# Optimization experiments

Hardware: AMD Instinct MI355X
Metric: run time of the kernel (lower is better)

Reference implementation:

```python
import jax, jax.numpy as jnp
import numpy as np
import math

EPS = 1e-6          # eps for safe cumprod / clamping
CHUNK = 4           # chunk_size w
SHARP = 1.0         # sharpening_factor
NOISE_STD = 1.0
N_HEADS = 4
ADIM = 512


def moving_sum(x, back, forward):
    """Windowed running sum over last axis: out[k] = sum_{j=k-back}^{k+forward} x[j].
    Equivalent to the conv1d trick in the original (all-ones filter)."""
    k = x.shape[-1]
    pad = [(0, 0)] * (x.ndim - 1) + [(back, forward)]
    c = jnp.cumsum(jnp.pad(x, pad), axis=-1)
    c0 = jnp.concatenate([jnp.zeros_like(c[..., :1]), c], axis=-1)
    w = back + forward
    return c0[..., w + 1: w + 1 + k] - c0[..., :k]


def setup_inputs() -> dict:
    rng = jax.random.key(0)
    ks = jax.random.split(rng, 12)
    B, qlen, klen, kdim, qdim, adim = 8, 256, 2048, 512, 512, ADIM
    s = 0.02
    return {
        "key_enc": jax.random.normal(ks[0], (B, klen, kdim), jnp.float32),
        "query":   jax.random.normal(ks[1], (B, qlen, qdim), jnp.float32),
        "noise":   jax.random.normal(ks[2], (B, qlen, klen), jnp.float32),
        # monotonic energy params
        "Wk_m": jax.random.normal(ks[3], (kdim, adim), jnp.float32) * s,
        "bk_m": jnp.zeros((adim,), jnp.float32),
        "Wq_m": jax.random.normal(ks[4], (qdim, adim), jnp.float32) * s,
        "bq_m": jnp.zeros((adim,), jnp.float32),
        "r":    jnp.array([-4.0], jnp.float32),
        # chunkwise energy params (multi-head)
        "Wk_c": jax.random.normal(ks[5], (kdim, adim), jnp.float32) * s,
        "bk_c": jnp.zeros((adim,), jnp.float32),
        "Wq_c": jax.random.normal(ks[6], (qdim, adim), jnp.float32) * s,
        "bq_c": jnp.zeros((adim,), jnp.float32),
    }


def _mocha_beta(key_enc, query, noise, Wk_m, bk_m, Wq_m, bq_m, r,
                Wk_c, bk_c, Wq_c, bq_c):
    B, klen, _ = key_enc.shape
    qlen = query.shape[1]
    H = N_HEADS
    dk = ADIM // H
    scale = math.sqrt(ADIM)

    # --- monotonic energy (single head): [B, qlen, klen]
    k_m = key_enc @ Wk_m + bk_m
    q_m = query @ Wq_m + bq_m
    e_mono = jnp.einsum('bqa,bka->bqk', q_m, k_m) / scale + r[0]

    # --- p_choose with additive gaussian noise (encourages discreteness)
    p_choose = jax.nn.sigmoid(e_mono + noise * NOISE_STD)  # [B,q,k]

    # --- safe cumprod of (1 - p) via exclusive cumsum in log space
    log1mp = jnp.log(jnp.clip(1.0 - p_choose, EPS, 1.0))
    cumprod_1mp = jnp.exp(jnp.cumsum(log1mp, axis=-1) - log1mp)  # exclusive

    # --- monotonic alpha recurrence over query steps (parallel-mode MoChA)
    aw0 = jnp.zeros((B, klen), jnp.float32).at[:, 0].set(1.0)

    def step(aw_prev, inp):
        p_i, cp_i = inp  # [B, klen]
        alpha_i = p_i * cp_i * jnp.cumsum(
            aw_prev / jnp.clip(cp_i, EPS, 1.0), axis=-1)
        return alpha_i, alpha_i

    xs = (jnp.swapaxes(p_choose, 0, 1), jnp.swapaxes(cumprod_1mp, 0, 1))
    _, alpha_q = jax.lax.scan(step, aw0, xs)          # [q, B, k]
    alpha = jnp.swapaxes(alpha_q, 0, 1)                # [B, q, k]

    # --- chunkwise energy (multi-head): [B, H, q, k]
    k_c = (key_enc @ Wk_c + bk_c).reshape(B, klen, H, dk)
    q_c = (query @ Wq_c + bq_c).reshape(B, qlen, H, dk)
    e_chunk = jnp.einsum('bqhd,bkhd->bhqk', q_c, k_c) / scale

    # --- efficient chunkwise attention (clipped-logit moving-sum softmax)
    e = e_chunk - jnp.max(e_chunk, axis=3, keepdims=True)
    softmax_exp = jnp.maximum(jnp.exp(e), 1e-5)
    denom = moving_sum(softmax_exp, back=CHUNK - 1, forward=0)
    beta = softmax_exp * moving_sum(
        alpha[:, None] * SHARP / denom, back=0, forward=CHUNK - 1)
    return beta  # [B, H, q, k]


def reference(key_enc, query, noise, Wk_m, bk_m, Wq_m, bq_m, r,
              Wk_c, bk_c, Wq_c, bq_c):
    return _mocha_beta(key_enc, query, noise, Wk_m, bk_m, Wq_m, bq_m, r,
                       Wk_c, bk_c, Wq_c, bq_c)
```

## Files before the change

### kernel.cpp

```cpp
#include <hip/hip_runtime.h>
#include <math.h>

#define BATCH   8
#define QLEN    256
#define KLEN    2048
#define KDIM    512
#define ADIMC   512
#define NHEADS  4
#define DKH     128
#define CHUNKW  4

static constexpr float INV_SCALE = 0.04419417382415922f;
static constexpr float EPSV = 1e-6f;

typedef __attribute__((ext_vector_type(8))) short bf16x8;
typedef __attribute__((ext_vector_type(4))) float f32x4;

__device__ __forceinline__ unsigned short f2bf(float f) {
    unsigned u = __builtin_bit_cast(unsigned, f);
    u += 0x7fffu + ((u >> 16) & 1u);
    return (unsigned short)(u >> 16);
}

__device__ __forceinline__ void lds_barrier() {
    __asm__ volatile("s_waitcnt lgkmcnt(0)\n\ts_barrier" ::: "memory");
}

__device__ __forceinline__ void gload_lds16(const void* g, void* l) {
    __builtin_amdgcn_global_load_lds(
        (const __attribute__((address_space(1))) void*)g,
        (__attribute__((address_space(3))) void*)l, 16, 0, 0);
}

#define NKXB (BATCH * KLEN * KDIM / 4 / 256)
#define NQXB (BATCH * QLEN * KDIM / 4 / 256)
__global__ __launch_bounds__(256) void prep(
    const float* __restrict__ key_enc, const float* __restrict__ query,
    const float* __restrict__ Wk_m, const float* __restrict__ Wk_c,
    const float* __restrict__ Wq_m, const float* __restrict__ Wq_c,
    unsigned short* __restrict__ kx, unsigned short* __restrict__ qx,
    unsigned short* __restrict__ WTk, unsigned short* __restrict__ WTq)
{
    __shared__ float tile[32][33];
    const int gb = blockIdx.x;
    const int tid = threadIdx.x;

    if (gb < NKXB + NQXB) {
        const float* x = (gb < NKXB) ? key_enc : query;
        unsigned short* y = (gb < NKXB) ? kx : qx;
        const int i = (gb < NKXB ? gb : gb - NKXB) * 256 + tid;
        float4 v = ((const float4*)x)[i];
        ushort4 o;
        o.x = f2bf(v.x); o.y = f2bf(v.y); o.z = f2bf(v.z); o.w = f2bf(v.w);
        ((ushort4*)y)[i] = o;
        return;
    }
    const int t = gb - NKXB - NQXB;
    const int which = t >> 8;
    const int tt = t & 255;
    const int bx = tt & 15, byy = tt >> 4;
    const float* W = (which == 0) ? Wk_m : (which == 1) ? Wk_c
                   : (which == 2) ? Wq_m : Wq_c;
    unsigned short* WT = (which == 0) ? WTk
                       : (which == 1) ? WTk + (size_t)512 * KDIM
                       : (which == 2) ? WTq : WTq + (size_t)512 * KDIM;
    const int tx = tid & 31, ty = tid >> 5;
    const int k0 = byy * 32, n0 = bx * 32;
    #pragma unroll
    for (int i = 0; i < 32; i += 8)
        tile[ty + i][tx] = W[(size_t)(k0 + ty + i) * KDIM + n0 + tx];
    __syncthreads();
    #pragma unroll
    for (int i = 0; i < 32; i += 8)
        WT[(size_t)(n0 + ty + i) * KDIM + k0 + tx] = f2bf(tile[tx][ty + i]);
}

template<int KSTEPS>
__device__ __forceinline__ void mfma_nt_staged(
    const unsigned short* __restrict__ A, const unsigned short* __restrict__ B,
    int lda, int ldb, int bm, int bn,
    unsigned short* AsLDS, unsigned short* BsLDS, f32x4 acc[4][4])
{
    const int t = threadIdx.x;
    const int wv = t >> 6, ln = t & 63;
    const int r = ln & 15, quad = ln >> 4;
    const int wm = (wv >> 1) * 64, wn = (wv & 1) * 64;
    const int srow = wv * 16 + (ln >> 2);
    const int scol = (ln & 3) * 8;

    for (int ks = 0; ks < KSTEPS; ++ks) {
        const int k0 = ks * 32;
        #pragma unroll
        for (int j = 0; j < 2; ++j) {
            gload_lds16(A + (size_t)(bm + j * 64 + srow) * lda + k0 + scol,
                        AsLDS + (size_t)(j * 64 + wv * 16) * 32);
            gload_lds16(B + (size_t)(bn + j * 64 + srow) * ldb + k0 + scol,
                        BsLDS + (size_t)(j * 64 + wv * 16) * 32);
        }
        __syncthreads();
        bf16x8 af[4], bg[4];
        #pragma unroll
        for (int f = 0; f < 4; ++f)
            af[f] = *(const bf16x8*)(AsLDS + (size_t)(wm + f * 16 + r) * 32 + quad * 8);
        #pragma unroll
        for (int f = 0; f < 4; ++f)
            bg[f] = *(const bf16x8*)(BsLDS + (size_t)(wn + f * 16 + r) * 32 + quad * 8);
        #pragma unroll
        for (int i = 0; i < 4; ++i)
            #pragma unroll
            for (int j2 = 0; j2 < 4; ++j2)
                acc[i][j2] = __builtin_amdgcn_mfma_f32_16x16x32_bf16(
                    af[i], bg[j2], acc[i][j2], 0, 0, 0);
        __syncthreads();
    }
}

__device__ __forceinline__ void zero_acc(f32x4 acc[4][4]) {
    #pragma unroll
    for (int i = 0; i < 4; ++i)
        #pragma unroll
        for (int j = 0; j < 4; ++j)
            acc[i][j] = f32x4{0.f, 0.f, 0.f, 0.f};
}

__global__ __launch_bounds__(256) void proj_mfma(
    const unsigned short* __restrict__ kx, const unsigned short* __restrict__ qx,
    const unsigned short* __restrict__ WTk, const unsigned short* __restrict__ WTq,
    const float* __restrict__ bk_m, const float* __restrict__ bk_c,
    const float* __restrict__ bq_m, const float* __restrict__ bq_c,
    unsigned short* __restrict__ kproj, unsigned short* __restrict__ qproj)
{
    __shared__ unsigned short As[128 * 32];
    __shared__ unsigned short Bs[128 * 32];
    const int by = blockIdx.y;
    const unsigned short *A, *WT;
    unsigned short* C;
    const float *bm_, *bc_;
    int bm;
    if (by < 128) { A = kx; WT = WTk; C = kproj; bm_ = bk_m; bc_ = bk_c; bm = by * 128; }
    else          { A = qx; WT = WTq; C = qproj; bm_ = bq_m; bc_ = bq_c; bm = (by - 128) * 128; }
    const int bn = blockIdx.x * 128;
    f32x4 acc[4][4]; zero_acc(acc);
    mfma_nt_staged<16>(A, WT, KDIM, KDIM, bm, bn, As, Bs, acc);
    const int wv = threadIdx.x >> 6, ln = threadIdx.x & 63;
    const int r = ln & 15, quad = ln >> 4;
    const int m0 = bm + (wv >> 1) * 64, n0 = bn + (wv & 1) * 64;
    #pragma unroll
    for (int j = 0; j < 4; ++j) {
        const int n = n0 + j * 16 + r;
        const float bv = (n < 512) ? bm_[n] : bc_[n - 512];
        #pragma unroll
        for (int i = 0; i < 4; ++i) {
            #pragma unroll
            for (int reg = 0; reg < 4; ++reg) {
                const int m = m0 + i * 16 + quad * 4 + reg;
                C[(size_t)m * 1024 + n] = f2bf(acc[i][j][reg] + bv);
            }
        }
    }
}

__global__ __launch_bounds__(256) void pchoose_mfma(
    const unsigned short* __restrict__ qp, const unsigned short* __restrict__ kp,
    const float* __restrict__ noise, const float* __restrict__ rp,
    float* __restrict__ p)
{
    __shared__ unsigned short As[128 * 32];
    __shared__ unsigned short Bs[128 * 32];
    const int b = blockIdx.z;
    const unsigned short* A = qp + (size_t)b * QLEN * 1024;
    const unsigned short* B = kp + (size_t)b * KLEN * 1024;
    const int bm = blockIdx.y * 128, bn = blockIdx.x * 128;
    f32x4 acc[4][4]; zero_acc(acc);
    mfma_nt_staged<16>(A, B, 1024, 1024, bm, bn, As, Bs, acc);
    const int wv = threadIdx.x >> 6, ln = threadIdx.x & 63;
    const int r = ln & 15, quad = ln >> 4;
    const int m0 = bm + (wv >> 1) * 64, n0 = bn + (wv & 1) * 64;
    const float rv = rp[0];
    #pragma unroll
    for (int i = 0; i < 4; ++i) {
        #pragma unroll
        for (int reg = 0; reg < 4; ++reg) {
            const int q = m0 + i * 16 + quad * 4 + reg;
            const size_t rowoff = ((size_t)b * QLEN + q) * KLEN;
            #pragma unroll
            for (int j = 0; j < 4; ++j) {
                const int k = n0 + j * 16 + r;
                const float e = acc[i][j][reg] * INV_SCALE + rv + noise[rowoff + k];
                p[rowoff + k] = __builtin_amdgcn_rcpf(1.0f + __expf(-e));
            }
        }
    }
}

__device__ __forceinline__ float wave_incl_scan(float x)
{
#define DPP_ADD(ctrl, rmask, bctrl)                                            \
    { int _t = __builtin_amdgcn_update_dpp(0, __builtin_bit_cast(int, x),      \
                                           ctrl, rmask, 0xf, bctrl);           \
      x += __builtin_bit_cast(float, _t); }
    DPP_ADD(0x111, 0xf, true)
    DPP_ADD(0x112, 0xf, true)
    DPP_ADD(0x114, 0xf, true)
    DPP_ADD(0x118, 0xf, true)
    DPP_ADD(0x142, 0xa, false)
    DPP_ADD(0x143, 0xc, false)
#undef DPP_ADD
    return x;
}

__global__ __launch_bounds__(256) void cumprod_mr(
    const float* __restrict__ p, float* __restrict__ mArr, float* __restrict__ rArr)
{
    const size_t row = blockIdx.x;
    const float* pr = p + row * KLEN;
    float* mr = mArr + row * KLEN;
    float* rr = rArr + row * KLEN;
    const int tid = threadIdx.x;
    const int lane = tid & 63, wid = tid >> 6;
    __shared__ float waveTot[4];

    float4 v0 = *(const float4*)(pr + tid * 8);
    float4 v1 = *(const float4*)(pr + tid * 8 + 4);
    float pv[8] = {v0.x, v0.y, v0.z, v0.w, v1.x, v1.y, v1.z, v1.w};
    float excl[8];
    float run = 0.0f;
    #pragma unroll
    for (int j = 0; j < 8; ++j) {
        float l = __logf(fminf(fmaxf(1.0f - pv[j], EPSV), 1.0f));
        excl[j] = run;
        run += l;
    }
    float s = wave_incl_scan(run);
    if (lane == 63) waveTot[wid] = s;
    __syncthreads();
    float wex = 0.0f;
    for (int w = 0; w < wid; ++w) wex += waveTot[w];
    const float texcl = wex + s - run;

    float mv[8], rv[8];
    #pragma unroll
    for (int j = 0; j < 8; ++j) {
        const float cpv = __expf(texcl + excl[j]);
        mv[j] = pv[j] * cpv;
        rv[j] = __builtin_amdgcn_rcpf(fminf(fmaxf(cpv, EPSV), 1.0f));
    }
    *(float4*)(mr + tid * 8)     = *(float4*)&mv[0];
    *(float4*)(mr + tid * 8 + 4) = *(float4*)&mv[4];
    *(float4*)(rr + tid * 8)     = *(float4*)&rv[0];
    *(float4*)(rr + tid * 8 + 4) = *(float4*)&rv[4];
}

__global__ __launch_bounds__(256, 1) void alpha_echunk(
    const float* __restrict__ mArr, const float* __restrict__ rArr,
    float* __restrict__ alpha,
    const unsigned short* __restrict__ qp, const unsigned short* __restrict__ kp,
    float* __restrict__ out)
{
    __shared__ __align__(16) char smem[98304];
    const int bid = blockIdx.x;
    const int tid = threadIdx.x;

    if (bid < BATCH) {
        __builtin_amdgcn_s_setprio(1);
        float (*wt)[4] = (float (*)[4])smem;
        const int lane = tid & 63, wid = tid >> 6;
        const float* mrow = mArr + (size_t)bid * QLEN * KLEN + tid * 8;
        const float* rrow = rArr + (size_t)bid * QLEN * KLEN + tid * 8;
        float* arow = alpha + (size_t)bid * QLEN * KLEN + tid * 8;

        float aw0 = 0.f, aw1 = 0.f, aw2 = 0.f, aw3 = 0.f;
        float aw4 = 0.f, aw5 = 0.f, aw6 = 0.f, aw7 = 0.f;
        if (tid == 0) aw0 = 1.0f;

        float4 mA0 = *(const float4*)(mrow);
        float4 mA1 = *(const float4*)(mrow + 4);
        float4 rA0 = *(const float4*)(rrow);
        float4 rA1 = *(const float4*)(rrow + 4);
        float4 mB0 = *(const float4*)(mrow + KLEN);
        float4 mB1 = *(const float4*)(mrow + KLEN + 4);
        float4 rB0 = *(const float4*)(rrow + KLEN);
        float4 rB1 = *(const float4*)(rrow + KLEN + 4);

#define ASTEP(I, M0, M1, R0, R1)                                               \
    {                                                                          \
        const int i_ = (I);                                                    \
        float4 mc0 = M0, mc1 = M1, rc0 = R0, rc1 = R1;                         \
        const int rn_ = (i_ + 2 < QLEN) ? (i_ + 2) : (QLEN - 1);               \
        M0 = *(const float4*)(mrow + (size_t)rn_ * KLEN);                      \
        M1 = *(const float4*)(mrow + (size_t)rn_ * KLEN + 4);                  \
        R0 = *(const float4*)(rrow + (size_t)rn_ * KLEN);                      \
        R1 = *(const float4*)(rrow + (size_t)rn_ * KLEN + 4);                  \
        float run = 0.0f, i0, i1, i2, i3, i4, i5, i6, i7;                      \
        run = fmaf(aw0, rc0.x, run); i0 = run;                                 \
        run = fmaf(aw1, rc0.y, run); i1 = run;                                 \
        run = fmaf(aw2, rc0.z, run); i2 = run;                                 \
        run = fmaf(aw3, rc0.w, run); i3 = run;                                 \
        run = fmaf(aw4, rc1.x, run); i4 = run;                                 \
        run = fmaf(aw5, rc1.y, run); i5 = run;                                 \
        run = fmaf(aw6, rc1.z, run); i6 = run;                                 \
        run = fmaf(aw7, rc1.w, run); i7 = run;                                 \
        float tot = wave_incl_scan(run);                                       \
        if (lane == 63) wt[i_ & 1][wid] = tot;                                 \
        lds_barrier();                                                         \
        float base = tot - run;                                                \
        float4 w0 = *(const float4*)&wt[i_ & 1][0];                            \
        if (wid > 0) base += w0.x;                                             \
        if (wid > 1) base += w0.y;                                             \
        if (wid > 2) base += w0.z;                                             \
        aw0 = mc0.x * (base + i0);                                             \
        aw1 = mc0.y * (base + i1);                                             \
        aw2 = mc0.z * (base + i2);                                             \
        aw3 = mc0.w * (base + i3);                                             \
        aw4 = mc1.x * (base + i4);                                             \
        aw5 = mc1.y * (base + i5);                                             \
        aw6 = mc1.z * (base + i6);                                             \
        aw7 = mc1.w * (base + i7);                                             \
        float4 ov0; ov0.x = aw0; ov0.y = aw1; ov0.z = aw2; ov0.w = aw3;        \
        float4 ov1; ov1.x = aw4; ov1.y = aw5; ov1.z = aw6; ov1.w = aw7;        \
        *(float4*)(arow + (size_t)i_ * KLEN)     = ov0;                        \
        *(float4*)(arow + (size_t)i_ * KLEN + 4) = ov1;                        \
    }

        for (int io = 0; io < QLEN; io += 2) {
            ASTEP(io + 0, mA0, mA1, rA0, rA1)
            ASTEP(io + 1, mB0, mB1, rB0, rB1)
        }
#undef ASTEP
        __builtin_amdgcn_s_setprio(0);
        return;
    }

    const int v = bid - BATCH;
    const int z = v >> 5;
    const int by = (v >> 4) & 1;
    const int bx = v & 15;
    const int b = z >> 2, h = z & 3;
    unsigned short* As = (unsigned short*)smem;
    unsigned short* Bs = (unsigned short*)(smem + 8192);
    const unsigned short* A = qp + (size_t)b * QLEN * 1024 + 512 + h * DKH;
    const unsigned short* B = kp + (size_t)b * KLEN * 1024 + 512 + h * DKH;
    const int bm = by * 128, bn = bx * 128;

    const int wv = tid >> 6, ln = tid & 63;
    const int r = ln & 15, quad = ln >> 4;
    const int wm = (wv >> 1) * 64, wn = (wv & 1) * 64;
    const int srow = wv * 16 + (ln >> 2);
    const int scol = (ln & 3) * 8;

    f32x4 acc[4][4]; zero_acc(acc);
    for (int ks = 0; ks < 4; ++ks) {
        const int k0 = ks * 32;
        #pragma unroll
        for (int j = 0; j < 2; ++j) {
            gload_lds16(A + (size_t)(bm + j * 64 + srow) * 1024 + k0 + scol,
                        As + (size_t)(j * 64 + wv * 16) * 32);
            gload_lds16(B + (size_t)(bn + j * 64 + srow) * 1024 + k0 + scol,
                        Bs + (size_t)(j * 64 + wv * 16) * 32);
        }
        __syncthreads();
        bf16x8 af[4], bg[4];
        #pragma unroll
        for (int f = 0; f < 4; ++f)
            af[f] = *(const bf16x8*)(As + (size_t)(wm + f * 16 + r) * 32 + quad * 8);
        #pragma unroll
        for (int f = 0; f < 4; ++f)
            bg[f] = *(const bf16x8*)(Bs + (size_t)(wn + f * 16 + r) * 32 + quad * 8);
        #pragma unroll
        for (int i = 0; i < 4; ++i)
            #pragma unroll
            for (int j2 = 0; j2 < 4; ++j2)
                acc[i][j2] = __builtin_amdgcn_mfma_f32_16x16x32_bf16(
                    af[i], bg[j2], acc[i][j2], 0, 0, 0);
        __syncthreads();
    }
    {
        const int m0 = bm + (wv >> 1) * 64, n0 = bn + (wv & 1) * 64;
        #pragma unroll
        for (int i = 0; i < 4; ++i) {
            #pragma unroll
            for (int reg = 0; reg < 4; ++reg) {
                const int q = m0 + i * 16 + quad * 4 + reg;
                const size_t rowoff = ((size_t)z * QLEN + q) * KLEN;
                #pragma unroll
                for (int j = 0; j < 4; ++j) {
                    const int k = n0 + j * 16 + r;
                    out[rowoff + k] = acc[i][j][reg] * INV_SCALE;
                }
            }
        }
    }
}

__global__ __launch_bounds__(256) void beta_kernel(
    float* __restrict__ eo, const float* __restrict__ alpha)
{
    __shared__ float sse[KLEN + 3];
    __shared__ float su[KLEN + 3];
    __shared__ float wmax[4];

    const int tid = threadIdx.x;
    const int lane = tid & 63, wid = tid >> 6;
    const int row = blockIdx.x;
    const int q = row & (QLEN - 1);
    const int b = row >> 10;
    float* erow = eo + (size_t)row * KLEN;
    const float* arow = alpha + ((size_t)b * QLEN + q) * KLEN;

    if (tid < 3) { sse[tid] = 0.0f; su[KLEN + tid] = 0.0f; }

    float ev[8];
    float lm = -INFINITY;
    #pragma unroll
    for (int j = 0; j < 8; ++j) {
        const int k = tid + 256 * j;
        ev[j] = erow[k];
        lm = fmaxf(lm, ev[j]);
    }
    #pragma unroll
    for (int off = 32; off > 0; off >>= 1) lm = fmaxf(lm, __shfl_xor(lm, off));
    if (lane == 0) wmax[wid] = lm;
    __syncthreads();
    const float mx = fmaxf(fmaxf(wmax[0], wmax[1]), fmaxf(wmax[2], wmax[3]));

    #pragma unroll
    for (int j = 0; j < 8; ++j) {
        const int k = tid + 256 * j;
        sse[k + 3] = fmaxf(__expf(ev[j] - mx), 1e-5f);
    }
    __syncthreads();

    #pragma unroll
    for (int j = 0; j < 8; ++j) {
        const int k = tid + 256 * j;
        const float denom = sse[k + 3] + sse[k + 2] + sse[k + 1] + sse[k];
        su[k] = arow[k] * __builtin_amdgcn_rcpf(denom);
    }
    __syncthreads();

    #pragma unroll
    for (int j = 0; j < 8; ++j) {
        const int k = tid + 256 * j;
        erow[k] = sse[k + 3] * (su[k] + su[k + 1] + su[k + 2] + su[k + 3]);
    }
}

extern "C" void kernel_launch(void* const* d_in, const int* in_sizes, int n_in,
                              void* d_out, int out_size, void* d_ws, size_t ws_size,
                              hipStream_t stream)
{
    (void)in_sizes; (void)n_in; (void)out_size; (void)ws_size;
    const float* key_enc = (const float*)d_in[0];
    const float* query   = (const float*)d_in[1];
    const float* noise   = (const float*)d_in[2];
    const float* Wk_m    = (const float*)d_in[3];
    const float* bk_m    = (const float*)d_in[4];
    const float* Wq_m    = (const float*)d_in[5];
    const float* bq_m    = (const float*)d_in[6];
    const float* rp      = (const float*)d_in[7];
    const float* Wk_c    = (const float*)d_in[8];
    const float* bk_c    = (const float*)d_in[9];
    const float* Wq_c    = (const float*)d_in[10];
    const float* bq_c    = (const float*)d_in[11];
    float* out = (float*)d_out;

    char* w = (char*)d_ws;
    unsigned short* kx    = (unsigned short*)w; w += (size_t)BATCH * KLEN * KDIM * 2;
    unsigned short* qx    = (unsigned short*)w; w += (size_t)BATCH * QLEN * KDIM * 2;
    unsigned short* WTk   = (unsigned short*)w; w += (size_t)1024 * KDIM * 2;
    unsigned short* WTq   = (unsigned short*)w; w += (size_t)1024 * KDIM * 2;
    unsigned short* kproj = (unsigned short*)w; w += (size_t)BATCH * KLEN * 1024 * 2;
    unsigned short* qproj = (unsigned short*)w; w += (size_t)BATCH * QLEN * 1024 * 2;
    float* p_alpha = (float*)w; w += (size_t)BATCH * QLEN * KLEN * 4;
    float* mArr    = (float*)w; w += (size_t)BATCH * QLEN * KLEN * 4;
    float* rArr    = (float*)w;

    hipLaunchKernelGGL(prep, dim3(NKXB + NQXB + 1024), dim3(256), 0, stream,
                       key_enc, query, Wk_m, Wk_c, Wq_m, Wq_c,
                       kx, qx, WTk, WTq);

    hipLaunchKernelGGL(proj_mfma, dim3(8, BATCH * KLEN / 128 + BATCH * QLEN / 128),
                       dim3(256), 0, stream,
                       kx, qx, WTk, WTq, bk_m, bk_c, bq_m, bq_c, kproj, qproj);

    hipLaunchKernelGGL(pchoose_mfma, dim3(KLEN / 128, QLEN / 128, BATCH), dim3(256), 0, stream,
                       qproj, kproj, noise, rp, p_alpha);

    hipLaunchKernelGGL(cumprod_mr, dim3(BATCH * QLEN), dim3(256), 0, stream,
                       p_alpha, mArr, rArr);

    hipLaunchKernelGGL(alpha_echunk, dim3(BATCH + KLEN / 128 * QLEN / 128 * BATCH * NHEADS),
                       dim3(256), 0, stream,
                       mArr, rArr, p_alpha, qproj, kproj, out);

    hipLaunchKernelGGL(beta_kernel, dim3(BATCH * NHEADS * QLEN), dim3(256), 0, stream,
                       out, p_alpha);
}
```

Measured before the change: 296.6 us.

## Widen alpha scan to 512 threads and software-pipeline the cross-wave prefix

The sequential alpha recurrence now runs with 512 threads, each holding 4 elements instead of 8. The scan is restructured so the block-level carry for step i is computed in step i-1 (a second wave scan publishes next-step partial sums to LDS), leaving one barrier per step with the slot read hoisted ahead. The GEMM blocks now launch 512 threads, and only the first 256 do any work. The intent is to shorten the serial per-step critical path. The cost is extra arithmetic and a second wave scan per step, and the GEMM part carries idle waves that lower occupancy.

```diff
diff --git a/kernel.cpp b/kernel.cpp
--- a/kernel.cpp
+++ b/kernel.cpp
@@ -251,7 +251,7 @@
     *(float4*)(rr + tid * 8 + 4) = *(float4*)&rv[4];
 }
 
-__global__ __launch_bounds__(256, 1) void alpha_echunk(
+__global__ __launch_bounds__(512, 1) void alpha_echunk(
     const float* __restrict__ mArr, const float* __restrict__ rArr,
     float* __restrict__ alpha,
     const unsigned short* __restrict__ qp, const unsigned short* __restrict__ kp,
@@ -263,68 +263,82 @@
 
     if (bid < BATCH) {
         __builtin_amdgcn_s_setprio(1);
-        float (*wt)[4] = (float (*)[4])smem;
+        float* slots = (float*)smem;
         const int lane = tid & 63, wid = tid >> 6;
-        const float* mrow = mArr + (size_t)bid * QLEN * KLEN + tid * 8;
-        const float* rrow = rArr + (size_t)bid * QLEN * KLEN + tid * 8;
-        float* arow = alpha + (size_t)bid * QLEN * KLEN + tid * 8;
-
-        float aw0 = 0.f, aw1 = 0.f, aw2 = 0.f, aw3 = 0.f;
-        float aw4 = 0.f, aw5 = 0.f, aw6 = 0.f, aw7 = 0.f;
-        if (tid == 0) aw0 = 1.0f;
-
-        float4 mA0 = *(const float4*)(mrow);
-        float4 mA1 = *(const float4*)(mrow + 4);
-        float4 rA0 = *(const float4*)(rrow);
-        float4 rA1 = *(const float4*)(rrow + 4);
-        float4 mB0 = *(const float4*)(mrow + KLEN);
-        float4 mB1 = *(const float4*)(mrow + KLEN + 4);
-        float4 rB0 = *(const float4*)(rrow + KLEN);
-        float4 rB1 = *(const float4*)(rrow + KLEN + 4);
-
-#define ASTEP(I, M0, M1, R0, R1)                                               \
+        const float* mrow = mArr + (size_t)bid * QLEN * KLEN + tid * 4;
+        const float* rrow = rArr + (size_t)bid * QLEN * KLEN + tid * 4;
+        float* arow = alpha + (size_t)bid * QLEN * KLEN + tid * 4;
+
+        float4 uP = *(const float4*)(rrow);
+        float4 mA = *(const float4*)(mrow);
+        float4 rA = *(const float4*)(rrow + KLEN);
+        float4 mB = *(const float4*)(mrow + KLEN);
+        float4 rB = *(const float4*)(rrow + 2 * KLEN);
+        float4 sP;
+        sP.x = (tid == 0) ? 1.0f : 0.0f; sP.y = 0.f; sP.z = 0.f; sP.w = 0.f;
+        float Cw = 0.0f;
+
+        if (tid < 16) slots[tid] = 0.0f;
+        lds_barrier();
+        if (tid == 0) slots[0] = uP.x;
+        lds_barrier();
+
+#define ASTEP(I, M, R)                                                         \
     {                                                                          \
         const int i_ = (I);                                                    \
-        float4 mc0 = M0, mc1 = M1, rc0 = R0, rc1 = R1;                         \
-        const int rn_ = (i_ + 2 < QLEN) ? (i_ + 2) : (QLEN - 1);               \
-        M0 = *(const float4*)(mrow + (size_t)rn_ * KLEN);                      \
-        M1 = *(const float4*)(mrow + (size_t)rn_ * KLEN + 4);                  \
-        R0 = *(const float4*)(rrow + (size_t)rn_ * KLEN);                      \
-        R1 = *(const float4*)(rrow + (size_t)rn_ * KLEN + 4);                  \
-        float run = 0.0f, i0, i1, i2, i3, i4, i5, i6, i7;                      \
-        run = fmaf(aw0, rc0.x, run); i0 = run;                                 \
-        run = fmaf(aw1, rc0.y, run); i1 = run;                                 \
-        run = fmaf(aw2, rc0.z, run); i2 = run;                                 \
-        run = fmaf(aw3, rc0.w, run); i3 = run;                                 \
-        run = fmaf(aw4, rc1.x, run); i4 = run;                                 \
-        run = fmaf(aw5, rc1.y, run); i5 = run;                                 \
-        run = fmaf(aw6, rc1.z, run); i6 = run;                                 \
-        run = fmaf(aw7, rc1.w, run); i7 = run;                                 \
-        float tot = wave_incl_scan(run);                                       \
-        if (lane == 63) wt[i_ & 1][wid] = tot;                                 \
+                 \
+        float4 t0 = *(const float4*)(slots + (i_ & 1) * 8);                    \
+        float4 t1 = *(const float4*)(slots + (i_ & 1) * 8 + 4);                \
+        float4 mc = M, rn = R;                                                 \
+        const int rm_ = (i_ + 2 < QLEN) ? (i_ + 2) : (QLEN - 1);               \
+        const int rr_ = (i_ + 3 < QLEN) ? (i_ + 3) : (QLEN - 1);               \
+        M = *(const float4*)(mrow + (size_t)rm_ * KLEN);                       \
+        R = *(const float4*)(rrow + (size_t)rr_ * KLEN);                       \
+             \
+        float c0 = uP.x * (Cw + sP.x);                                         \
+        float c1 = fmaf(uP.y, Cw + sP.y, c0);                                  \
+        float c2 = fmaf(uP.z, Cw + sP.z, c1);                                  \
+        float c3 = fmaf(uP.w, Cw + sP.w, c2);                                  \
+        const float runx = c3;                                                 \
+        const float scx = wave_incl_scan(runx);                                \
+                    \
+        float Ci = 0.0f;                                                       \
+        if (wid > 0) Ci += t0.x;                                               \
+        if (wid > 1) Ci += t0.y;                                               \
+        if (wid > 2) Ci += t0.z;                                               \
+        if (wid > 3) Ci += t0.w;                                               \
+        if (wid > 4) Ci += t1.x;                                               \
+        if (wid > 5) Ci += t1.y;                                               \
+        if (wid > 6) Ci += t1.z;                                               \
+                                                        \
+        float4 u;                                                              \
+        u.x = mc.x * rn.x; u.y = mc.y * rn.y;                                  \
+        u.z = mc.z * rn.z; u.w = mc.w * rn.w;                                  \
+                                                            \
+        const float bb = Ci + (scx - runx);                                    \
+        const float G0 = bb + c0, G1 = bb + c1, G2 = bb + c2, G3 = bb + c3;    \
+           \
+        float ys = u.x * G0;                                                   \
+        ys = fmaf(u.y, G1, ys);                                                \
+        ys = fmaf(u.z, G2, ys);                                                \
+        ys = fmaf(u.w, G3, ys);                                                \
+        const float sy = wave_incl_scan(ys);                                   \
+        if (lane == 63) slots[((i_ + 1) & 1) * 8 + wid] = sy;                  \
+                                                             \
+        float4 ov;                                                             \
+        ov.x = mc.x * G0; ov.y = mc.y * G1;                                    \
+        ov.z = mc.z * G2; ov.w = mc.w * G3;                                    \
+        *(float4*)(arow + (size_t)i_ * KLEN) = ov;                             \
+                                                             \
+        const float sb = scx - runx;                                           \
+        sP.x = sb + c0; sP.y = sb + c1; sP.z = sb + c2; sP.w = sb + c3;        \
+        uP = u; Cw = Ci;                                                       \
         lds_barrier();                                                         \
-        float base = tot - run;                                                \
-        float4 w0 = *(const float4*)&wt[i_ & 1][0];                            \
-        if (wid > 0) base += w0.x;                                             \
-        if (wid > 1) base += w0.y;                                             \
-        if (wid > 2) base += w0.z;                                             \
-        aw0 = mc0.x * (base + i0);                                             \
-        aw1 = mc0.y * (base + i1);                                             \
-        aw2 = mc0.z * (base + i2);                                             \
-        aw3 = mc0.w * (base + i3);                                             \
-        aw4 = mc1.x * (base + i4);                                             \
-        aw5 = mc1.y * (base + i5);                                             \
-        aw6 = mc1.z * (base + i6);                                             \
-        aw7 = mc1.w * (base + i7);                                             \
-        float4 ov0; ov0.x = aw0; ov0.y = aw1; ov0.z = aw2; ov0.w = aw3;        \
-        float4 ov1; ov1.x = aw4; ov1.y = aw5; ov1.z = aw6; ov1.w = aw7;        \
-        *(float4*)(arow + (size_t)i_ * KLEN)     = ov0;                        \
-        *(float4*)(arow + (size_t)i_ * KLEN + 4) = ov1;                        \
     }
 
         for (int io = 0; io < QLEN; io += 2) {
-            ASTEP(io + 0, mA0, mA1, rA0, rA1)
-            ASTEP(io + 1, mB0, mB1, rB0, rB1)
+            ASTEP(io + 0, mA, rA)
+            ASTEP(io + 1, mB, rB)
         }
 #undef ASTEP
         __builtin_amdgcn_s_setprio(0);
@@ -336,6 +350,7 @@
     const int by = (v >> 4) & 1;
     const int bx = v & 15;
     const int b = z >> 2, h = z & 3;
+    const bool worker = tid < 256;
     unsigned short* As = (unsigned short*)smem;
     unsigned short* Bs = (unsigned short*)(smem + 8192);
     const unsigned short* A = qp + (size_t)b * QLEN * 1024 + 512 + h * DKH;
@@ -345,36 +360,40 @@
     const int wv = tid >> 6, ln = tid & 63;
     const int r = ln & 15, quad = ln >> 4;
     const int wm = (wv >> 1) * 64, wn = (wv & 1) * 64;
-    const int srow = wv * 16 + (ln >> 2);
+    const int srow = (wv & 3) * 16 + (ln >> 2);
     const int scol = (ln & 3) * 8;
 
     f32x4 acc[4][4]; zero_acc(acc);
     for (int ks = 0; ks < 4; ++ks) {
         const int k0 = ks * 32;
-        #pragma unroll
-        for (int j = 0; j < 2; ++j) {
-            gload_lds16(A + (size_t)(bm + j * 64 + srow) * 1024 + k0 + scol,
-                        As + (size_t)(j * 64 + wv * 16) * 32);
-            gload_lds16(B + (size_t)(bn + j * 64 + srow) * 1024 + k0 + scol,
-                        Bs + (size_t)(j * 64 + wv * 16) * 32);
+        if (worker) {
+            #pragma unroll
+            for (int j = 0; j < 2; ++j) {
+                gload_lds16(A + (size_t)(bm + j * 64 + srow) * 1024 + k0 + scol,
+                            As + (size_t)(j * 64 + wv * 16) * 32);
+                gload_lds16(B + (size_t)(bn + j * 64 + srow) * 1024 + k0 + scol,
+                            Bs + (size_t)(j * 64 + wv * 16) * 32);
+            }
         }
         __syncthreads();
-        bf16x8 af[4], bg[4];
-        #pragma unroll
-        for (int f = 0; f < 4; ++f)
-            af[f] = *(const bf16x8*)(As + (size_t)(wm + f * 16 + r) * 32 + quad * 8);
-        #pragma unroll
-        for (int f = 0; f < 4; ++f)
-            bg[f] = *(const bf16x8*)(Bs + (size_t)(wn + f * 16 + r) * 32 + quad * 8);
-        #pragma unroll
-        for (int i = 0; i < 4; ++i)
-            #pragma unroll
-            for (int j2 = 0; j2 < 4; ++j2)
-                acc[i][j2] = __builtin_amdgcn_mfma_f32_16x16x32_bf16(
-                    af[i], bg[j2], acc[i][j2], 0, 0, 0);
+        if (worker) {
+            bf16x8 af[4], bg[4];
+            #pragma unroll
+            for (int f = 0; f < 4; ++f)
+                af[f] = *(const bf16x8*)(As + (size_t)(wm + f * 16 + r) * 32 + quad * 8);
+            #pragma unroll
+            for (int f = 0; f < 4; ++f)
+                bg[f] = *(const bf16x8*)(Bs + (size_t)(wn + f * 16 + r) * 32 + quad * 8);
+            #pragma unroll
+            for (int i = 0; i < 4; ++i)
+                #pragma unroll
+                for (int j2 = 0; j2 < 4; ++j2)
+                    acc[i][j2] = __builtin_amdgcn_mfma_f32_16x16x32_bf16(
+                        af[i], bg[j2], acc[i][j2], 0, 0, 0);
+        }
         __syncthreads();
     }
-    {
+    if (worker) {
         const int m0 = bm + (wv >> 1) * 64, n0 = bn + (wv & 1) * 64;
         #pragma unroll
         for (int i = 0; i < 4; ++i) {
@@ -490,7 +509,7 @@
                        p_alpha, mArr, rArr);
 
     hipLaunchKernelGGL(alpha_echunk, dim3(BATCH + KLEN / 128 * QLEN / 128 * BATCH * NHEADS),
-                       dim3(256), 0, stream,
+                       dim3(512), 0, stream,
                        mArr, rArr, p_alpha, qproj, kproj, out);
 
     hipLaunchKernelGGL(beta_kernel, dim3(BATCH * NHEADS * QLEN), dim3(256), 0, stream,
```

Result: slower. 307.7 us (+3.7%).
